# Kernel optimization log

Hardware: AMD Instinct MI355X
Metric: run time of the kernel (lower is better)

## Reference

```python
import jax, jax.numpy as jnp
import numpy as np

BN_EPS = 1e-5
LN_EPS = 1e-5


def conv1d(x, w, b):
    # x: (B, Cin, L), w: (Cout, Cin, K) 'same' padding
    pad = (w.shape[-1] - 1) // 2
    y = jax.lax.conv_general_dilated(x, w, (1,), [(pad, pad)],
                                     dimension_numbers=('NCH', 'OIH', 'NCH'))
    return y + b[None, :, None]


def bn_eval(x, g, b):
    # BatchNorm1d in eval mode with running_mean=0, running_var=1
    scale = g / np.float32(np.sqrt(1.0 + BN_EPS))
    return x * scale[None, :, None] + b[None, :, None]


def dss_kernel(lam_re, lam_im, log_dt, W_re, W_im, L):
    # lam_*: (N,), log_dt: (H,), W_*: (2, H, N) -> K: (2, H, L) real
    Lam = -jnp.exp(lam_re) + 1j * lam_im                  # (N,) stable poles
    dt = jnp.exp(log_dt)                                   # (H,)
    dtL = dt[:, None] * Lam[None, :]                       # (H, N)
    # ZOH-style input discretization folded into W
    Wc = (W_re + 1j * W_im) * ((jnp.exp(dtL) - 1.0) / Lam[None, :])[None]  # (2,H,N)
    pos = jnp.arange(L, dtype=jnp.float32)
    E = jnp.exp(dtL[:, :, None] * pos[None, None, :])      # (H, N, L) complex Vandermonde
    return jnp.einsum('chn,hnl->chl', Wc, E).real          # (2, H, L)


def dss_layer(x, lam_re, lam_im, log_dt, W_re, W_im, D, out_w, out_b):
    # x: (B, H, L) transposed DSS block, bidirectional, postact='glu'
    B, H, L = x.shape
    K = dss_kernel(lam_re, lam_im, log_dt, W_re, W_im, L)  # (2, H, L)
    zpad = jnp.zeros_like(K[0])
    k = (jnp.concatenate([K[0], zpad], -1) +
         jnp.concatenate([zpad, K[1][..., ::-1]], -1))     # (H, 2L) bidirectional kernel
    k_f = jnp.fft.rfft(k, axis=-1)                          # (H, L+1)
    u_f = jnp.fft.rfft(x, n=2 * L, axis=-1)                 # (B, H, L+1)
    y = jnp.fft.irfft(k_f[None] * u_f, n=2 * L, axis=-1)[..., :L]
    y = y + D[None, :, None] * x                            # skip term
    y = jax.nn.gelu(y, approximate=False)
    y = jnp.einsum('oh,bhl->bol', out_w, y) + out_b[None, :, None]  # (B, 2H, L)
    a, g = jnp.split(y, 2, axis=1)
    return a * jax.nn.sigmoid(g)                            # GLU -> (B, H, L)


def layernorm_ch(x, g, b):
    # LayerNorm over channel dim of (B, H, L)
    mu = x.mean(axis=1, keepdims=True)
    var = ((x - mu) ** 2).mean(axis=1, keepdims=True)
    return (x - mu) / jnp.sqrt(var + LN_EPS) * g[None, :, None] + b[None, :, None]


def reference(x, enc_w, enc_b, rn_w1, rn_b1, rn_g1, rn_be1, rn_w2, rn_b2, rn_g2,
              rn_be2, lam_re, lam_im, log_dt, W_re, W_im, D, out_w, out_b,
              ln_g, ln_b, dec_w, dec_b):
    x = conv1d(x, enc_w, enc_b)                             # (B, H, L)
    for i in range(rn_w1.shape[0]):                         # resnet L1Blocks
        z = jax.nn.relu(bn_eval(conv1d(x, rn_w1[i], rn_b1[i]), rn_g1[i], rn_be1[i]))
        z = bn_eval(conv1d(z, rn_w2[i], rn_b2[i]), rn_g2[i], rn_be2[i])
        x = jax.nn.relu(z + x)
    for i in range(lam_re.shape[0]):                        # DSS blocks (post-norm)
        z = dss_layer(x, lam_re[i], lam_im[i], log_dt[i], W_re[i], W_im[i],
                      D[i], out_w[i], out_b[i])
        x = layernorm_ch(z + x, ln_g[i], ln_b[i])
    return conv1d(x, dec_w, dec_b)                          # (B, d_output, L)


def setup_inputs() -> dict:
    key = jax.random.key(0)
    ks = jax.random.split(key, 12)
    B, L, H, N = 16, 8192, 128, 32
    nl, nr = 4, 3
    f = lambda k, shape, s=1.0: jax.random.normal(k, shape, dtype=jnp.float32) * np.float32(s)
    x = f(ks[0], (B, 5, L))
    enc_w = f(ks[1], (H, 5, 15), 1.0 / np.sqrt(5 * 15)); enc_b = jnp.zeros((H,), jnp.float32)
    rn_w1 = f(ks[2], (nr, H, H, 7), 1.0 / np.sqrt(H * 7)); rn_b1 = jnp.zeros((nr, H), jnp.float32)
    rn_w2 = f(ks[3], (nr, H, H, 7), 1.0 / np.sqrt(H * 7)); rn_b2 = jnp.zeros((nr, H), jnp.float32)
    rn_g1 = jnp.ones((nr, H), jnp.float32); rn_be1 = jnp.zeros((nr, H), jnp.float32)
    rn_g2 = jnp.ones((nr, H), jnp.float32); rn_be2 = jnp.zeros((nr, H), jnp.float32)
    lam_re = f(ks[4], (nl, N), 0.5)
    lam_im = jnp.pi * jnp.arange(N, dtype=jnp.float32)[None, :] * jnp.ones((nl, 1), jnp.float32)
    log_dt = f(ks[5], (nl, H), 0.5) - 4.0
    W_re = f(ks[6], (nl, 2, H, N), 1.0 / np.sqrt(N))
    W_im = f(ks[7], (nl, 2, H, N), 1.0 / np.sqrt(N))
    D = f(ks[8], (nl, H))
    out_w = f(ks[9], (nl, 2 * H, H), 1.0 / np.sqrt(H)); out_b = jnp.zeros((nl, 2 * H), jnp.float32)
    ln_g = jnp.ones((nl, H), jnp.float32); ln_b = jnp.zeros((nl, H), jnp.float32)
    dec_w = f(ks[10], (5, H, 15), 1.0 / np.sqrt(H * 15)); dec_b = jnp.zeros((5,), jnp.float32)
    return {'x': x, 'enc_w': enc_w, 'enc_b': enc_b, 'rn_w1': rn_w1, 'rn_b1': rn_b1,
            'rn_g1': rn_g1, 'rn_be1': rn_be1, 'rn_w2': rn_w2, 'rn_b2': rn_b2,
            'rn_g2': rn_g2, 'rn_be2': rn_be2, 'lam_re': lam_re, 'lam_im': lam_im,
            'log_dt': log_dt, 'W_re': W_re, 'W_im': W_im, 'D': D, 'out_w': out_w,
            'out_b': out_b, 'ln_g': ln_g, 'ln_b': ln_b, 'dec_w': dec_w, 'dec_b': dec_b}
```

## Files before the change

### kernel.cpp

```cpp
#include <hip/hip_runtime.h>
#include <hip/hip_bf16.h>


#define BN   16
#define HCH  128
#define LSEQ 8192
#define NST  32
#define NLAY 4
#define XT_BSTRIDE 2101248ull

typedef __attribute__((ext_vector_type(4))) float f32x4;
typedef __attribute__((ext_vector_type(8))) short short8;
typedef unsigned short u16;
typedef unsigned int   u32;

struct __align__(8) U2 { u32 x, y; };
struct __align__(16) US8 { u16 v[8]; };

__device__ __forceinline__ u16 f2bf(float f){
  union { float f; u32 u; } v; v.f = f;
  u32 u = v.u;
  return (u16)((u + 0x7fffu + ((u >> 16) & 1u)) >> 16);
}
__device__ __forceinline__ float bf2f(u32 lo16){
  union { u32 u; float f; } v; v.u = lo16 << 16; return v.f;
}
__device__ __forceinline__ float geluf(float v){
  return 0.5f * v * (1.0f + erff(v * 0.70710678118654752f));
}

#define GLDS16(g, l) \
  __builtin_amdgcn_global_load_lds((const __attribute__((address_space(1))) u32*)(g), \
                                   (__attribute__((address_space(3))) u32*)(l), 16, 0, 0)

__global__ void k_xpad(u16* xTs){
  int b = blockIdx.x, t = threadIdx.x;
  char* base = (char*)xTs + (size_t)b * XT_BSTRIDE;
  int r = t >> 4;
  int row = (r < 8) ? r : (8192 + r);
  f32x4 z = {0.f, 0.f, 0.f, 0.f};
  *(f32x4*)(base + (size_t)row * 256 + (size_t)(t & 15) * 16) = z;
}

__global__ void k_wxform(const float* __restrict__ w1, const float* __restrict__ w2, u16* __restrict__ wswz){
  int idx = blockIdx.x * 256 + threadIdx.x;
  if (idx >= 6 * 128 * 896) return;
  int conv = idx / (128 * 896);
  int rem  = idx % (128 * 896);
  int co = rem / 896, K = rem % 896;
  int k = K >> 7, ci = K & 127;
  const float* src = (conv & 1) ? w2 : w1;
  int blk = conv >> 1;
  float v = src[(((size_t)blk * 128 + co) * 128 + ci) * 7 + k];
  int chunk = K >> 6, j = K & 63;
  size_t byteoff = (size_t)conv * 229376 + (size_t)chunk * 16384 + (size_t)co * 128
                 + (u32)((j * 2) ^ ((co & 7) << 4));
  *(u16*)((char*)wswz + byteoff) = f2bf(v);
}

__global__ void k_wdec(const float* __restrict__ dw, u16* __restrict__ wd){
  int idx = blockIdx.x * 256 + threadIdx.x;
  if (idx >= 16 * 1920) return;
  int co = idx / 1920, K = idx % 1920;
  int k = K >> 7, ci = K & 127;
  float v = (co < 5) ? dw[((size_t)co * 128 + ci) * 15 + k] : 0.f;
  size_t byteoff = (size_t)co * 3840 + (u32)((K * 2) ^ ((co & 7) << 4));
  *(u16*)((char*)wd + byteoff) = f2bf(v);
}

__global__ void k_wglu(const float* __restrict__ ow, u16* __restrict__ wg){
  int idx = blockIdx.x * 256 + threadIdx.x;
  if (idx >= NLAY * 256 * 128) return;
  int layer = idx >> 15;
  int rem = idx & 32767;
  int q = rem >> 7, k = rem & 127;
  int row = (q & 1) ? (128 + (q >> 1)) : (q >> 1);
  float v = ow[((size_t)layer * 256 + row) * 128 + k];
  u16 hb = f2bf(v);
  u16 lb = f2bf(v - bf2f(hb));
  int a_hi = k >> 6, kk = k & 63;
  size_t base = (size_t)layer * 131072 + (size_t)q * 128 + (u32)((kk * 2) ^ ((q & 7) << 4));
  *(u16*)((char*)wg + base + (size_t)a_hi * 32768) = hb;
  *(u16*)((char*)wg + base + (size_t)(2 + a_hi) * 32768) = lb;
}

__global__ void k_dssprep(const float* __restrict__ lam_re, const float* __restrict__ lam_im,
                          const float* __restrict__ log_dt, const float* __restrict__ W_re,
                          const float* __restrict__ W_im, float* __restrict__ dssp){
  int idx = blockIdx.x * 256 + threadIdx.x;
  if (idx >= NLAY * HCH * NST) return;
  int layer = idx / (HCH * NST);
  int hn = idx % (HCH * NST);
  int h = hn / NST, n = hn % NST;
  float Lre = -expf(lam_re[layer * NST + n]);
  float Lim = lam_im[layer * NST + n];
  float dt  = expf(log_dt[layer * HCH + h]);
  float are = dt * Lre, aim = dt * Lim;
  float er = expf(are);
  float rre = er * cosf(aim);
  float rim = er * sinf(aim);
  float nre = rre - 1.f, nim = rim;
  float den = 1.f / (Lre * Lre + Lim * Lim);
  float fre = (nre * Lre + nim * Lim) * den;
  float fim = (nim * Lre - nre * Lim) * den;
  float* base = dssp + (size_t)layer * 6 * HCH * NST;
  base[(0 * HCH + h) * NST + n] = rre;
  base[(1 * HCH + h) * NST + n] = rim;
  #pragma unroll
  for (int cc = 0; cc < 2; ++cc){
    float wr_ = W_re[(((size_t)layer * 2 + cc) * HCH + h) * NST + n];
    float wi_ = W_im[(((size_t)layer * 2 + cc) * HCH + h) * NST + n];
    base[((2 + 2 * cc) * HCH + h) * NST + n] = wr_ * fre - wi_ * fim;
    base[((3 + 2 * cc) * HCH + h) * NST + n] = wr_ * fim + wi_ * fre;
  }
}

__global__ __launch_bounds__(256) void k_mats(const float* __restrict__ pp,
                                              u16* __restrict__ A1c, u16* __restrict__ A2c,
                                              float* __restrict__ rC){
  int h = blockIdx.x, t = threadIdx.x;
  __shared__ float pre[129][33], pim[129][33];
  __shared__ float w0re[32], w0im[32], w1re[32], w1im[32];
  __shared__ float tf[128], tb[128];
  if (t < 32){
    int n = t;
    float rre = pp[(0 * HCH + h) * NST + n], rim = pp[(1 * HCH + h) * NST + n];
    w0re[n] = pp[(2 * HCH + h) * NST + n]; w0im[n] = pp[(3 * HCH + h) * NST + n];
    w1re[n] = pp[(4 * HCH + h) * NST + n]; w1im[n] = pp[(5 * HCH + h) * NST + n];
    float pr = 1.f, pi = 0.f;
    pre[0][n] = 1.f; pim[0][n] = 0.f;
    for (int p = 1; p <= 128; ++p){
      float nr = pr * rre - pi * rim;
      float ni = pr * rim + pi * rre;
      pr = nr; pi = ni;
      pre[p][n] = pr; pim[p][n] = pi;
    }
    rC[h * 64 + 2 * n] = pr; rC[h * 64 + 2 * n + 1] = pi;
  }
  __syncthreads();
  if (t < 128){
    float s = 0.f;
    for (int n = 0; n < 32; ++n) s += w0re[n] * pre[t][n] - w0im[n] * pim[t][n];
    tf[t] = s;
  } else {
    int d = t - 128;
    if (d == 0) tb[0] = 0.f;
    else {
      float s = 0.f;
      for (int n = 0; n < 32; ++n) s += w1re[n] * pre[d - 1][n] - w1im[n] * pim[d - 1][n];
      tb[d] = s;
    }
  }
  __syncthreads();
  for (int idx = t; idx < 4 * 128 * 64; idx += 256){
    int a = idx >> 13, rem = idx & 8191, q = rem >> 6, k = rem & 63;
    int j = (a & 1) * 64 + k;
    int n, p; float wr_, wi_;
    if (q < 64){ n = q >> 1; p = 127 - j; wr_ = w0re[n]; wi_ = w0im[n]; }
    else       { n = (q - 64) >> 1; p = j; wr_ = w1re[n]; wi_ = w1im[n]; }
    float pr = pre[p][n], pi = pim[p][n];
    float v = (q & 1) ? (wr_ * pi + wi_ * pr) : (wr_ * pr - wi_ * pi);
    u16 hb = f2bf(v);
    u16 ob = (a < 2) ? hb : f2bf(v - bf2f(hb));
    *(u16*)((char*)A1c + (size_t)h * 65536 + (size_t)a * 16384 + (size_t)q * 128
            + (u32)((k * 2) ^ ((q & 7) << 4))) = ob;
  }
  for (int idx = t; idx < 8 * 128 * 64; idx += 256){
    int a = idx >> 13, rem = idx & 8191, i = rem >> 6, k = rem & 63;
    float v; bool lo;
    if (a < 4){
      int colT = (a & 1) * 64 + k;
      v = (i >= colT) ? tf[i - colT] : tb[colT - i];
      lo = (a >= 2);
    } else {
      int n = k >> 1;
      int p = (a < 6) ? (i + 1) : (127 - i);
      v = (k & 1) ? -pim[p][n] : pre[p][n];
      lo = (a == 5) || (a == 7);
    }
    u16 hb = f2bf(v);
    u16 ob = lo ? f2bf(v - bf2f(hb)) : hb;
    *(u16*)((char*)A2c + (size_t)h * 131072 + (size_t)a * 16384 + (size_t)i * 128
            + (u32)((k * 2) ^ ((i & 7) << 4))) = ob;
  }
}

__global__ __launch_bounds__(128) void k_enc(const float* __restrict__ xin, const float* __restrict__ w,
                                             const float* __restrict__ bias, float* __restrict__ X){
  int b = blockIdx.y, l0 = blockIdx.x * 64;
  int t = threadIdx.x;
  __shared__ float xs[5][78];
  for (int i = t; i < 5 * 78; i += 128){
    int ci = i / 78, j = i % 78;
    int l = l0 - 7 + j;
    xs[ci][j] = (l >= 0 && l < LSEQ) ? xin[((size_t)b * 5 + ci) * LSEQ + l] : 0.f;
  }
  float wreg[75];
  #pragma unroll
  for (int i = 0; i < 75; ++i) wreg[i] = w[t * 75 + i];
  float bc = bias[t];
  __syncthreads();
  size_t orow = ((size_t)b * HCH + t) * LSEQ + l0;
  for (int gb = 0; gb < 8; ++gb){
    float acc[8] = {0, 0, 0, 0, 0, 0, 0, 0};
    #pragma unroll
    for (int ci = 0; ci < 5; ++ci){
      #pragma unroll
      for (int k = 0; k < 15; ++k){
        float wv = wreg[ci * 15 + k];
        #pragma unroll
        for (int j = 0; j < 8; ++j)
          acc[j] = fmaf(wv, xs[ci][gb * 8 + j + k], acc[j]);
      }
    }
    f32x4 o0 = {acc[0] + bc, acc[1] + bc, acc[2] + bc, acc[3] + bc};
    f32x4 o1 = {acc[4] + bc, acc[5] + bc, acc[6] + bc, acc[7] + bc};
    *(f32x4*)&X[orow + gb * 8]     = o0;
    *(f32x4*)&X[orow + gb * 8 + 4] = o1;
  }
}

__global__ __launch_bounds__(256) void k_xform(const float* __restrict__ Xin, u16* __restrict__ xTs){
  int b = blockIdx.y, l0 = blockIdx.x * 64;
  int t = threadIdx.x;
  __shared__ float tile[128][65];
  #pragma unroll
  for (int it = 0; it < 32; ++it){
    int idx = t + it * 256;
    int ci = idx >> 6, j = idx & 63;
    tile[ci][j] = Xin[((size_t)b * HCH + ci) * LSEQ + l0 + j];
  }
  __syncthreads();
  int rl = t >> 2, q = t & 3;
  int l = l0 + rl;
  char* rowp = (char*)xTs + (size_t)b * XT_BSTRIDE + (size_t)(l + 8) * 256;
  u32 key = ((u32)l & 7u) << 4;
  #pragma unroll
  for (int ii = 0; ii < 8; ++ii){
    int c0 = q * 32 + ii * 4;
    U2 val;
    val.x = (u32)f2bf(tile[c0 + 0][rl]) | ((u32)f2bf(tile[c0 + 1][rl]) << 16);
    val.y = (u32)f2bf(tile[c0 + 2][rl]) | ((u32)f2bf(tile[c0 + 3][rl]) << 16);
    *(U2*)(rowp + (((u32)(c0 * 2)) ^ key)) = val;
  }
}

__global__ __launch_bounds__(256, 2) void k_conv(
    const u16* __restrict__ xTs, const u16* __restrict__ wcv,
    const float* __restrict__ bng, const float* __restrict__ bnb, const float* __restrict__ bnbe,
    const float* __restrict__ Xres, float* __restrict__ Xout)
{
  int b = blockIdx.y, l0 = blockIdx.x * 128;
  int tid = threadIdx.x, lane = tid & 63, wv = tid >> 6;
  int wr = wv >> 1, wc = wv & 1;
  int lan15 = lane & 15, lhi = lane >> 4;

  __shared__ alignas(16) u16 xt[144 * 128];
  __shared__ alignas(16) u16 wch[2][128 * 64];

  const char* xsrc = (const char*)xTs + (size_t)b * XT_BSTRIDE + (size_t)l0 * 256;
  #pragma unroll
  for (int is = 0; is < 9; ++is){
    int off = is * 4096 + wv * 1024;
    GLDS16(xsrc + off + (lane << 4), (char*)xt + off);
  }
  {
    const char* wsrc = (const char*)wcv;
    #pragma unroll
    for (int is = 0; is < 4; ++is){
      int off = is * 4096 + wv * 1024;
      GLDS16(wsrc + off + (lane << 4), (char*)&wch[0][0] + off);
    }
  }
  asm volatile("s_waitcnt vmcnt(0)" ::: "memory");
  __syncthreads();

  f32x4 acc[4][4];
  #pragma unroll
  for (int i = 0; i < 4; ++i)
    #pragma unroll
    for (int j = 0; j < 4; ++j) acc[i][j] = (f32x4){0.f, 0.f, 0.f, 0.f};

  for (int c = 0; c < 14; ++c){
    int cur = c & 1;
    if (c < 13){
      const char* wsrc = (const char*)wcv + (size_t)(c + 1) * 16384;
      #pragma unroll
      for (int is = 0; is < 4; ++is){
        int off = is * 4096 + wv * 1024;
        GLDS16(wsrc + off + (lane << 4), (char*)&wch[cur ^ 1][0] + off);
      }
    }
    int k = c >> 1;
    const char* wb = (const char*)&wch[cur][0];
    #pragma unroll
    for (int ks = 0; ks < 2; ++ks){
      short8 af[4], bf[4];
      int j0 = ks * 32 + lhi * 8;
      #pragma unroll
      for (int mt = 0; mt < 4; ++mt){
        int co = wr * 64 + mt * 16 + lan15;
        af[mt] = *(const short8*)(wb + co * 128 + ((j0 * 2) ^ ((co & 7) << 4)));
      }
      int ci0 = (c & 1) * 64 + ks * 32 + lhi * 8;
      #pragma unroll
      for (int nt = 0; nt < 4; ++nt){
        int ll = wc * 64 + nt * 16 + lan15;
        int row = ll + k + 5;
        int lg = l0 + ll + k - 3;
        bf[nt] = *(const short8*)((const char*)xt + row * 256 + ((ci0 * 2) ^ ((lg & 7) << 4)));
      }
      #pragma unroll
      for (int mt = 0; mt < 4; ++mt)
        #pragma unroll
        for (int nt = 0; nt < 4; ++nt)
          acc[mt][nt] = __builtin_amdgcn_mfma_f32_16x16x32_bf16(af[mt], bf[nt], acc[mt][nt], 0, 0, 0);
    }
    asm volatile("s_waitcnt vmcnt(0)" ::: "memory");
    __syncthreads();
  }

  bool hasres = (Xres != nullptr);
  #pragma unroll
  for (int mt = 0; mt < 4; ++mt){
    #pragma unroll
    for (int reg = 0; reg < 4; ++reg){
      int co = wr * 64 + mt * 16 + (lhi << 2) + reg;
      float A = bng[co] * 0.99999500003749968f;
      float Bc = fmaf(bnb[co], A, bnbe[co]);
      size_t rowb = ((size_t)b * HCH + co) * LSEQ;
      #pragma unroll
      for (int nt = 0; nt < 4; ++nt){
        int l = l0 + wc * 64 + nt * 16 + lan15;
        float v = fmaf(acc[mt][nt][reg], A, Bc);
        if (hasres) v += Xres[rowb + l];
        v = fmaxf(v, 0.f);
        Xout[rowb + l] = v;
      }
    }
  }
}

__device__ __forceinline__ void stage_x_tile(const float* __restrict__ X, int h, int ct,
                                             char* xh, char* xl, int t){
  int k8 = t & 15;
  int c0 = t >> 4;
  #pragma unroll
  for (int it = 0; it < 8; ++it){
    int col = c0 + it * 16;
    int c = ct * 8 + (col >> 4), b = col & 15;
    const float* src = X + ((size_t)b * HCH + h) * LSEQ + (size_t)c * 128 + k8 * 8;
    f32x4 v0 = *(const f32x4*)src;
    f32x4 v1 = *(const f32x4*)(src + 4);
    US8 hi, lo;
    #pragma unroll
    for (int e = 0; e < 4; ++e){
      u16 hb = f2bf(v0[e]);
      hi.v[e] = hb; lo.v[e] = f2bf(v0[e] - bf2f(hb));
      u16 hb2 = f2bf(v1[e]);
      hi.v[e + 4] = hb2; lo.v[e + 4] = f2bf(v1[e] - bf2f(hb2));
    }
    u32 off = (u32)col * 256 + (u32)((k8 * 16) ^ ((col & 7) << 4));
    *(US8*)(xh + off) = hi;
    *(US8*)(xl + off) = lo;
  }
}

__global__ __launch_bounds__(256) void k_dss1(const float* __restrict__ X,
                                              const u16* __restrict__ A1c,
                                              float* __restrict__ P){
  int ct = blockIdx.x, h = blockIdx.y;
  int tid = threadIdx.x, lane = tid & 63, wv = tid >> 6;
  int wr = wv >> 1, wc = wv & 1, lan15 = lane & 15, lhi = lane >> 4;
  __shared__ alignas(16) u16 bx[32768];
  __shared__ alignas(16) u16 ach[2][8192];

  stage_x_tile(X, h, ct, (char*)bx, (char*)bx + 32768, tid);
  const char* abase = (const char*)A1c + (size_t)h * 65536;
  #pragma unroll
  for (int is = 0; is < 4; ++is){
    int off = is * 4096 + wv * 1024;
    GLDS16(abase + off + (lane << 4), (char*)&ach[0][0] + off);
  }
  asm volatile("s_waitcnt vmcnt(0)" ::: "memory");
  __syncthreads();

  f32x4 acc[4][4];
  #pragma unroll
  for (int i = 0; i < 4; ++i)
    #pragma unroll
    for (int j = 0; j < 4; ++j) acc[i][j] = (f32x4){0.f, 0.f, 0.f, 0.f};

  const int asel[6] = {0, 1, 0, 1, 2, 3};
  const int bsel[6] = {0, 0, 1, 1, 0, 0};
  const int bk0 [6] = {0, 64, 0, 64, 0, 64};
  #pragma unroll
  for (int s = 0; s < 6; ++s){
    if (s < 5){
      const char* an = abase + (size_t)asel[s + 1] * 16384;
      #pragma unroll
      for (int is = 0; is < 4; ++is){
        int off = is * 4096 + wv * 1024;
        GLDS16(an + off + (lane << 4), (char*)&ach[(s + 1) & 1][0] + off);
      }
    }
    const char* bt = (const char*)bx + bsel[s] * 32768;
    const char* at = (const char*)&ach[s & 1][0];
    #pragma unroll
    for (int ks = 0; ks < 2; ++ks){
      int ka = ks * 32 + lhi * 8;
      short8 af[4], bf[4];
      #pragma unroll
      for (int mt = 0; mt < 4; ++mt){
        int q = wr * 64 + mt * 16 + lan15;
        af[mt] = *(const short8*)(at + q * 128 + ((ka * 2) ^ ((q & 7) << 4)));
      }
      int kb = bk0[s] + ka;
      #pragma unroll
      for (int nt = 0; nt < 4; ++nt){
        int col = wc * 64 + nt * 16 + lan15;
        bf[nt] = *(const short8*)(bt + col * 256 + ((kb * 2) ^ ((col & 7) << 4)));
      }
      #pragma unroll
      for (int mt = 0; mt < 4; ++mt)
        #pragma unroll
        for (int nt = 0; nt < 4; ++nt)
          acc[mt][nt] = __builtin_amdgcn_mfma_f32_16x16x32_bf16(af[mt], bf[nt], acc[mt][nt], 0, 0, 0);
    }
    asm volatile("s_waitcnt vmcnt(0)" ::: "memory");
    __syncthreads();
  }

  #pragma unroll
  for (int mt = 0; mt < 4; ++mt)
    #pragma unroll
    for (int nt = 0; nt < 4; ++nt){
      int col = ct * 128 + wc * 64 + nt * 16 + lan15;
      int q0 = wr * 64 + mt * 16 + (lhi << 2);
      *(f32x4*)&P[((size_t)h * 1024 + col) * 128 + q0] = acc[mt][nt];
    }
}

__global__ __launch_bounds__(256) void k_scan(const float* __restrict__ P,
                                              const float* __restrict__ rC,
                                              u16* __restrict__ Sf, u16* __restrict__ Sb){
  int part = blockIdx.x & 3, h = blockIdx.x >> 2;
  int t = threadIdx.x;
  int dir = part >> 1;
  int b = (part & 1) * 8 + (t >> 5);
  int n = t & 31;
  float rre = rC[h * 64 + 2 * n], rim = rC[h * 64 + 2 * n + 1];
  u16* SO = dir ? Sb : Sf;
  const float* pbase = P + (size_t)h * 131072 + (size_t)b * 128 + dir * 64 + 2 * n;
  float sre = 0.f, sim = 0.f;
  u32 key = ((u32)b & 7u) << 4;
  for (int ii = 0; ii < 64; ++ii){
    int c = dir ? (63 - ii) : ii;
    u16 hr = f2bf(sre), hm = f2bf(sim);
    u32 hw = (u32)hr | ((u32)hm << 16);
    u32 lw = (u32)f2bf(sre - bf2f(hr)) | ((u32)f2bf(sim - bf2f(hm)) << 16);
    char* sp = (char*)SO + ((size_t)(h * 8 + (c >> 3)) * 2) * 16384
             + (size_t)((c & 7) * 16 + b) * 128 + (u32)((4 * n) ^ key);
    *(u32*)sp = hw;
    *(u32*)(sp + 16384) = lw;
    const float* pp = pbase + (size_t)c * 2048;
    float pr = pp[0], pi = pp[1];
    float nr = rre * sre - rim * sim + pr;
    float ni = rre * sim + rim * sre + pi;
    sre = nr; sim = ni;
  }
}

__global__ __launch_bounds__(256) void k_dss2(const float* __restrict__ X,
                                              const u16* __restrict__ A2c,
                                              const u16* __restrict__ Sf,
                                              const u16* __restrict__ Sb,
                                              const float* __restrict__ Dv,
                                              float* __restrict__ G){
  int ct = blockIdx.x, h = blockIdx.y;
  int tid = threadIdx.x, lane = tid & 63, wv = tid >> 6;
  int wr = wv >> 1, wc = wv & 1, lan15 = lane & 15, lhi = lane >> 4;
  __shared__ alignas(16) u16 bx[32768];
  __shared__ alignas(16) u16 ach[2][8192];

  stage_x_tile(X, h, ct, (char*)bx, (char*)bx + 32768, tid);
  const char* abase = (const char*)A2c + (size_t)h * 131072;
  #pragma unroll
  for (int is = 0; is < 4; ++is){
    int off = is * 4096 + wv * 1024;
    GLDS16(abase + off + (lane << 4), (char*)&ach[0][0] + off);
  }
  asm volatile("s_waitcnt vmcnt(0)" ::: "memory");
  __syncthreads();

  f32x4 acc[4][4];
  #pragma unroll
  for (int i = 0; i < 4; ++i)
    #pragma unroll
    for (int j = 0; j < 4; ++j) acc[i][j] = (f32x4){0.f, 0.f, 0.f, 0.f};

  {
    const int asel[6] = {0, 1, 0, 1, 2, 3};
    const int bsel[6] = {0, 0, 1, 1, 0, 0};
    const int bk0 [6] = {0, 64, 0, 64, 0, 64};
    #pragma unroll
    for (int s = 0; s < 6; ++s){
      if (s < 5){
        const char* an = abase + (size_t)asel[s + 1] * 16384;
        #pragma unroll
        for (int is = 0; is < 4; ++is){
          int off = is * 4096 + wv * 1024;
          GLDS16(an + off + (lane << 4), (char*)&ach[(s + 1) & 1][0] + off);
        }
      }
      const char* bt = (const char*)bx + bsel[s] * 32768;
      const char* at = (const char*)&ach[s & 1][0];
      #pragma unroll
      for (int ks = 0; ks < 2; ++ks){
        int ka = ks * 32 + lhi * 8;
        short8 af[4], bf[4];
        #pragma unroll
        for (int mt = 0; mt < 4; ++mt){
          int i = wr * 64 + mt * 16 + lan15;
          af[mt] = *(const short8*)(at + i * 128 + ((ka * 2) ^ ((i & 7) << 4)));
        }
        int kb = bk0[s] + ka;
        #pragma unroll
        for (int nt = 0; nt < 4; ++nt){
          int col = wc * 64 + nt * 16 + lan15;
          bf[nt] = *(const short8*)(bt + col * 256 + ((kb * 2) ^ ((col & 7) << 4)));
        }
        #pragma unroll
        for (int mt = 0; mt < 4; ++mt)
          #pragma unroll
          for (int nt = 0; nt < 4; ++nt)
            acc[mt][nt] = __builtin_amdgcn_mfma_f32_16x16x32_bf16(af[mt], bf[nt], acc[mt][nt], 0, 0, 0);
      }
      asm volatile("s_waitcnt vmcnt(0)" ::: "memory");
      __syncthreads();
    }
  }
  {
    const char* st0 = (const char*)Sf + ((size_t)(h * 8 + ct) * 2) * 16384;
    const char* st2 = (const char*)Sb + ((size_t)(h * 8 + ct) * 2) * 16384;
    const char* stile[4] = {st0, st0 + 16384, st2, st2 + 16384};
    #pragma unroll
    for (int tt = 0; tt < 4; ++tt){
      #pragma unroll
      for (int is = 0; is < 4; ++is){
        int off = is * 4096 + wv * 1024;
        GLDS16(stile[tt] + off + (lane << 4), (char*)bx + tt * 16384 + off);
      }
    }
    const char* an = abase + 4 * 16384;
    #pragma unroll
    for (int is = 0; is < 4; ++is){
      int off = is * 4096 + wv * 1024;
      GLDS16(an + off + (lane << 4), (char*)&ach[0][0] + off);
    }
    asm volatile("s_waitcnt vmcnt(0)" ::: "memory");
    __syncthreads();
  }
  {
    const int asel[6] = {4, 4, 5, 6, 6, 7};
    const int bof [6] = {0, 16384, 0, 32768, 49152, 32768};
    #pragma unroll
    for (int s = 0; s < 6; ++s){
      if (s < 5){
        const char* an = abase + (size_t)asel[s + 1] * 16384;
        #pragma unroll
        for (int is = 0; is < 4; ++is){
          int off = is * 4096 + wv * 1024;
          GLDS16(an + off + (lane << 4), (char*)&ach[(s + 1) & 1][0] + off);
        }
      }
      const char* bt = (const char*)bx + bof[s];
      const char* at = (const char*)&ach[s & 1][0];
      #pragma unroll
      for (int ks = 0; ks < 2; ++ks){
        int ka = ks * 32 + lhi * 8;
        short8 af[4], bf[4];
        #pragma unroll
        for (int mt = 0; mt < 4; ++mt){
          int i = wr * 64 + mt * 16 + lan15;
          af[mt] = *(const short8*)(at + i * 128 + ((ka * 2) ^ ((i & 7) << 4)));
        }
        #pragma unroll
        for (int nt = 0; nt < 4; ++nt){
          int col = wc * 64 + nt * 16 + lan15;
          bf[nt] = *(const short8*)(bt + col * 128 + ((ka * 2) ^ ((col & 7) << 4)));
        }
        #pragma unroll
        for (int mt = 0; mt < 4; ++mt)
          #pragma unroll
          for (int nt = 0; nt < 4; ++nt)
            acc[mt][nt] = __builtin_amdgcn_mfma_f32_16x16x32_bf16(af[mt], bf[nt], acc[mt][nt], 0, 0, 0);
      }
      asm volatile("s_waitcnt vmcnt(0)" ::: "memory");
      __syncthreads();
    }
  }
  float Dh = Dv[h];
  #pragma unroll
  for (int mt = 0; mt < 4; ++mt)
    #pragma unroll
    for (int nt = 0; nt < 4; ++nt){
      int col = wc * 64 + nt * 16 + lan15;
      int c = ct * 8 + (col >> 4), b = col & 15;
      int i0 = wr * 64 + mt * 16 + (lhi << 2);
      size_t base = ((size_t)b * HCH + h) * LSEQ + (size_t)c * 128 + i0;
      f32x4 xv = *(const f32x4*)&X[base];
      f32x4 ov;
      #pragma unroll
      for (int e = 0; e < 4; ++e)
        ov[e] = geluf(acc[mt][nt][e] + Dh * xv[e]);
      *(f32x4*)&G[base] = ov;
    }
}

__global__ __launch_bounds__(256) void k_glu2(
    const float* __restrict__ G,
    const u16* __restrict__ Wg,
    const float* __restrict__ ob,
    const float* __restrict__ lng, const float* __restrict__ lnb,
    float* __restrict__ X)
{
  int b = blockIdx.y, l0 = blockIdx.x * 64;
  int tid = threadIdx.x, lane = tid & 63, wv = tid >> 6;
  int lan15 = lane & 15, lhi = lane >> 4;
  __shared__ alignas(16) u16 gt[2][64 * 128];
  __shared__ alignas(16) u16 ach[256 * 64];
  __shared__ float lnbuf[4][64][2];

  {
    int hp = tid & 63, lgrp = tid >> 6;
    const float* g0 = G + ((size_t)b * HCH + 2 * hp) * LSEQ + l0 + lgrp * 16;
    const float* g1 = g0 + LSEQ;
    #pragma unroll
    for (int j4 = 0; j4 < 4; ++j4){
      f32x4 r0 = *(const f32x4*)(g0 + j4 * 4);
      f32x4 r1 = *(const f32x4*)(g1 + j4 * 4);
      #pragma unroll
      for (int e = 0; e < 4; ++e){
        int l = lgrp * 16 + j4 * 4 + e;
        u16 h0 = f2bf(r0[e]), h1 = f2bf(r1[e]);
        u16 q0 = f2bf(r0[e] - bf2f(h0)), q1 = f2bf(r1[e] - bf2f(h1));
        u32 off = (u32)l * 256 + (((u32)hp * 4) ^ (((u32)l & 7u) << 4));
        *(u32*)((char*)&gt[0][0] + off) = (u32)h0 | ((u32)h1 << 16);
        *(u32*)((char*)&gt[1][0] + off) = (u32)q0 | ((u32)q1 << 16);
      }
    }
  }

  f32x4 acc[4][4];
  #pragma unroll
  for (int i = 0; i < 4; ++i)
    #pragma unroll
    for (int j = 0; j < 4; ++j) acc[i][j] = (f32x4){0.f, 0.f, 0.f, 0.f};

  const int asel[6] = {0, 1, 0, 1, 2, 3};
  const int bsel[6] = {0, 0, 1, 1, 0, 0};
  const int bk0 [6] = {0, 64, 0, 64, 0, 64};
  for (int s = 0; s < 6; ++s){
    __syncthreads();
    const char* an = (const char*)Wg + (size_t)asel[s] * 32768;
    #pragma unroll
    for (int is = 0; is < 8; ++is){
      int off = is * 4096 + wv * 1024;
      GLDS16(an + off + (lane << 4), (char*)ach + off);
    }
    asm volatile("s_waitcnt vmcnt(0)" ::: "memory");
    __syncthreads();
    const char* bt = (const char*)&gt[bsel[s]][0];
    #pragma unroll
    for (int ks = 0; ks < 2; ++ks){
      int ka = ks * 32 + lhi * 8;
      short8 af[4], bf[4];
      #pragma unroll
      for (int mt = 0; mt < 4; ++mt){
        int q = wv * 64 + mt * 16 + lan15;
        af[mt] = *(const short8*)((const char*)ach + q * 128 + ((ka * 2) ^ ((q & 7) << 4)));
      }
      int kb = bk0[s] + ka;
      #pragma unroll
      for (int nt = 0; nt < 4; ++nt){
        int col = nt * 16 + lan15;
        bf[nt] = *(const short8*)(bt + col * 256 + ((kb * 2) ^ ((col & 7) << 4)));
      }
      #pragma unroll
      for (int mt = 0; mt < 4; ++mt)
        #pragma unroll
        for (int nt = 0; nt < 4; ++nt)
          acc[mt][nt] = __builtin_amdgcn_mfma_f32_16x16x32_bf16(af[mt], bf[nt], acc[mt][nt], 0, 0, 0);
    }
  }

  float s1v[4] = {0, 0, 0, 0}, s2v[4] = {0, 0, 0, 0};
  float oba[4][2], obg[4][2];
  #pragma unroll
  for (int mt = 0; mt < 4; ++mt)
    #pragma unroll
    for (int e = 0; e < 2; ++e){
      int o = wv * 32 + mt * 8 + lhi * 2 + e;
      oba[mt][e] = ob[o]; obg[mt][e] = ob[o + 128];
    }
  #pragma unroll
  for (int nt = 0; nt < 4; ++nt){
    int l = l0 + nt * 16 + lan15;
    #pragma unroll
    for (int mt = 0; mt < 4; ++mt){
      #pragma unroll
      for (int e = 0; e < 2; ++e){
        int o = wv * 32 + mt * 8 + lhi * 2 + e;
        float a = acc[mt][nt][2 * e]     + oba[mt][e];
        float g = acc[mt][nt][2 * e + 1] + obg[mt][e];
        float z = a * (1.f / (1.f + expf(-g)));
        float u = z + X[((size_t)b * HCH + o) * LSEQ + l];
        acc[mt][nt][2 * e] = u;
        s1v[nt] += u; s2v[nt] += u * u;
      }
    }
  }
  #pragma unroll
  for (int nt = 0; nt < 4; ++nt){
    s1v[nt] += __shfl_xor(s1v[nt], 16, 64);
    s1v[nt] += __shfl_xor(s1v[nt], 32, 64);
    s2v[nt] += __shfl_xor(s2v[nt], 16, 64);
    s2v[nt] += __shfl_xor(s2v[nt], 32, 64);
  }
  if (lhi == 0){
    #pragma unroll
    for (int nt = 0; nt < 4; ++nt){
      lnbuf[wv][nt * 16 + lan15][0] = s1v[nt];
      lnbuf[wv][nt * 16 + lan15][1] = s2v[nt];
    }
  }
  __syncthreads();
  #pragma unroll
  for (int nt = 0; nt < 4; ++nt){
    int col = nt * 16 + lan15;
    float S1 = lnbuf[0][col][0] + lnbuf[1][col][0] + lnbuf[2][col][0] + lnbuf[3][col][0];
    float S2 = lnbuf[0][col][1] + lnbuf[1][col][1] + lnbuf[2][col][1] + lnbuf[3][col][1];
    float mu = S1 * (1.f / 128.f);
    float var = S2 * (1.f / 128.f) - mu * mu;
    float rs = rsqrtf(var + 1e-5f);
    int l = l0 + col;
    #pragma unroll
    for (int mt = 0; mt < 4; ++mt)
      #pragma unroll
      for (int e = 0; e < 2; ++e){
        int o = wv * 32 + mt * 8 + lhi * 2 + e;
        float u = acc[mt][nt][2 * e];
        X[((size_t)b * HCH + o) * LSEQ + l] = (u - mu) * rs * lng[o] + lnb[o];
      }
  }
}

__global__ __launch_bounds__(256, 1) void k_dec2(const u16* __restrict__ xTs, const u16* __restrict__ wd,
                                                 const float* __restrict__ bias, float* __restrict__ out){
  int b = blockIdx.y, l0 = blockIdx.x * 128;
  int tid = threadIdx.x, lane = tid & 63, wv = tid >> 6;
  int lan15 = lane & 15, lhi = lane >> 4;
  __shared__ alignas(16) u16 xt[144 * 128];
  __shared__ alignas(16) u16 ws[16 * 1920];
  const char* xsrc = (const char*)xTs + (size_t)b * XT_BSTRIDE + (size_t)l0 * 256;
  #pragma unroll
  for (int is = 0; is < 9; ++is){
    int off = is * 4096 + wv * 1024;
    GLDS16(xsrc + off + (lane << 4), (char*)xt + off);
  }
  #pragma unroll
  for (int is = 0; is < 15; ++is){
    int off = is * 4096 + wv * 1024;
    GLDS16((const char*)wd + off + (lane << 4), (char*)ws + off);
  }
  asm volatile("s_waitcnt vmcnt(0)" ::: "memory");
  __syncthreads();
  f32x4 acc[2] = {(f32x4){0, 0, 0, 0}, (f32x4){0, 0, 0, 0}};
  for (int k = 0; k < 15; ++k){
    #pragma unroll
    for (int ks = 0; ks < 4; ++ks){
      int K = k * 128 + ks * 32 + lhi * 8;
      short8 af = *(const short8*)((const char*)ws + lan15 * 3840 + (((u32)(K * 2)) ^ (((u32)lan15 & 7u) << 4)));
      #pragma unroll
      for (int nt = 0; nt < 2; ++nt){
        int ll = wv * 32 + nt * 16 + lan15;
        int lg = l0 + ll + k - 7;
        int row = ll + k + 1;
        short8 bf = *(const short8*)((const char*)xt + row * 256 + ((((ks * 32 + lhi * 8) * 2)) ^ ((lg & 7) << 4)));
        acc[nt] = __builtin_amdgcn_mfma_f32_16x16x32_bf16(af, bf, acc[nt], 0, 0, 0);
      }
    }
  }
  #pragma unroll
  for (int nt = 0; nt < 2; ++nt){
    int l = l0 + wv * 32 + nt * 16 + lan15;
    #pragma unroll
    for (int reg = 0; reg < 4; ++reg){
      int co = (lhi << 2) + reg;
      if (co < 5) out[((size_t)b * 5 + co) * LSEQ + l] = acc[nt][reg] + bias[co];
    }
  }
}

extern "C" void kernel_launch(void* const* d_in, const int* in_sizes, int n_in,
                              void* d_out, int out_size, void* d_ws, size_t ws_size,
                              hipStream_t stream){
  (void)in_sizes; (void)n_in; (void)out_size; (void)ws_size;
  const float* x_in   = (const float*)d_in[0];
  const float* enc_w  = (const float*)d_in[1];
  const float* enc_b  = (const float*)d_in[2];
  const float* rn_w1  = (const float*)d_in[3];
  const float* rn_b1  = (const float*)d_in[4];
  const float* rn_g1  = (const float*)d_in[5];
  const float* rn_be1 = (const float*)d_in[6];
  const float* rn_w2  = (const float*)d_in[7];
  const float* rn_b2  = (const float*)d_in[8];
  const float* rn_g2  = (const float*)d_in[9];
  const float* rn_be2 = (const float*)d_in[10];
  const float* lam_re = (const float*)d_in[11];
  const float* lam_im = (const float*)d_in[12];
  const float* log_dt = (const float*)d_in[13];
  const float* W_re   = (const float*)d_in[14];
  const float* W_im   = (const float*)d_in[15];
  const float* Dv     = (const float*)d_in[16];
  const float* out_w  = (const float*)d_in[17];
  const float* out_b  = (const float*)d_in[18];
  const float* ln_g   = (const float*)d_in[19];
  const float* ln_b   = (const float*)d_in[20];
  const float* dec_w  = (const float*)d_in[21];
  const float* dec_b  = (const float*)d_in[22];

  char* ws = (char*)d_ws;
  float* X    = (float*)(ws + 0ull);
  float* PG   = (float*)(ws + 67108864ull);
  u16*   Sf   = (u16*)  (ws + 134217728ull);
  u16*   Sb   = (u16*)  (ws + 167772160ull);
  u16*   xTs  = (u16*)  (ws + 134217728ull);
  u16*   A1c  = (u16*)  (ws + 201326592ull);
  u16*   A2c  = (u16*)  (ws + 209715200ull);
  u16*   wswz = (u16*)  (ws + 226492416ull);
  u16*   wdec = (u16*)  (ws + 227868672ull);
  float* dssp = (float*)(ws + 227930112ull);
  float* rC   = (float*)(ws + 228323328ull);
  u16*   wglu = (u16*)  (ws + 228356096ull);

  k_xpad<<<16, 256, 0, stream>>>(xTs);
  k_wxform<<<2688, 256, 0, stream>>>(rn_w1, rn_w2, wswz);
  k_wdec<<<120, 256, 0, stream>>>(dec_w, wdec);
  k_wglu<<<512, 256, 0, stream>>>(out_w, wglu);
  k_dssprep<<<64, 256, 0, stream>>>(lam_re, lam_im, log_dt, W_re, W_im, dssp);
  k_enc<<<dim3(128, 16), 128, 0, stream>>>(x_in, enc_w, enc_b, X);

  for (int r = 0; r < 3; ++r){
    k_xform<<<dim3(128, 16), 256, 0, stream>>>(X, xTs);
    k_conv<<<dim3(64, 16), 256, 0, stream>>>(xTs, (const u16*)((char*)wswz + (size_t)(2 * r) * 229376),
        rn_g1 + r * HCH, rn_b1 + r * HCH, rn_be1 + r * HCH, nullptr, PG);
    k_xform<<<dim3(128, 16), 256, 0, stream>>>(PG, xTs);
    k_conv<<<dim3(64, 16), 256, 0, stream>>>(xTs, (const u16*)((char*)wswz + (size_t)(2 * r + 1) * 229376),
        rn_g2 + r * HCH, rn_b2 + r * HCH, rn_be2 + r * HCH, X, X);
  }
  for (int dl = 0; dl < NLAY; ++dl){
    k_mats<<<128, 256, 0, stream>>>(dssp + (size_t)dl * 6 * HCH * NST, A1c, A2c, rC);
    k_dss1<<<dim3(8, 128), 256, 0, stream>>>(X, A1c, PG);
    k_scan<<<512, 256, 0, stream>>>(PG, rC, Sf, Sb);
    k_dss2<<<dim3(8, 128), 256, 0, stream>>>(X, A2c, Sf, Sb, Dv + dl * HCH, PG);
    k_glu2<<<dim3(128, 16), 256, 0, stream>>>(PG, (const u16*)((char*)wglu + (size_t)dl * 131072),
        out_b + dl * 256, ln_g + dl * HCH, ln_b + dl * HCH, X);
  }
  k_xpad<<<16, 256, 0, stream>>>(xTs);
  k_xform<<<dim3(128, 16), 256, 0, stream>>>(X, xTs);
  k_dec2<<<dim3(64, 16), 256, 0, stream>>>(xTs, wdec, dec_b, (float*)d_out);
}
```

Measured before the change: 1.744 ms.

## Fuse bf16 transpose into conv epilogue, restructure DSS GEMM staging and grid order

```diff
diff --git a/kernel.cpp b/kernel.cpp
--- a/kernel.cpp
+++ b/kernel.cpp
@@ -16,6 +16,7 @@
 
 struct __align__(8) U2 { u32 x, y; };
 struct __align__(16) US8 { u16 v[8]; };
+struct __align__(8) US4 { u16 v[4]; };
 
 __device__ __forceinline__ u16 f2bf(float f){
   union { float f; u32 u; } v; v.f = f;
@@ -248,7 +249,7 @@
 __global__ __launch_bounds__(256, 2) void k_conv(
     const u16* __restrict__ xTs, const u16* __restrict__ wcv,
     const float* __restrict__ bng, const float* __restrict__ bnb, const float* __restrict__ bnbe,
-    const float* __restrict__ Xres, float* __restrict__ Xout)
+    const float* __restrict__ Xres, float* __restrict__ Xout, u16* __restrict__ xTsOut)
 {
   int b = blockIdx.y, l0 = blockIdx.x * 128;
   int tid = threadIdx.x, lane = tid & 63, wv = tid >> 6;
@@ -321,23 +322,41 @@
   }
 
   bool hasres = (Xres != nullptr);
+  bool hasout = (Xout != nullptr);
+  u16* tr = xt;
   #pragma unroll
   for (int mt = 0; mt < 4; ++mt){
+    float A4[4], B4[4];
+    int co0 = wr * 64 + mt * 16 + (lhi << 2);
     #pragma unroll
     for (int reg = 0; reg < 4; ++reg){
-      int co = wr * 64 + mt * 16 + (lhi << 2) + reg;
-      float A = bng[co] * 0.99999500003749968f;
-      float Bc = fmaf(bnb[co], A, bnbe[co]);
-      size_t rowb = ((size_t)b * HCH + co) * LSEQ;
-      #pragma unroll
-      for (int nt = 0; nt < 4; ++nt){
-        int l = l0 + wc * 64 + nt * 16 + lan15;
-        float v = fmaf(acc[mt][nt][reg], A, Bc);
-        if (hasres) v += Xres[rowb + l];
+      A4[reg] = bng[co0 + reg] * 0.99999500003749968f;
+      B4[reg] = fmaf(bnb[co0 + reg], A4[reg], bnbe[co0 + reg]);
+    }
+    #pragma unroll
+    for (int nt = 0; nt < 4; ++nt){
+      int ll = wc * 64 + nt * 16 + lan15;
+      int l = l0 + ll;
+      US4 o;
+      #pragma unroll
+      for (int reg = 0; reg < 4; ++reg){
+        float v = fmaf(acc[mt][nt][reg], A4[reg], B4[reg]);
+        if (hasres) v += Xres[((size_t)b * HCH + co0 + reg) * LSEQ + l];
         v = fmaxf(v, 0.f);
-        Xout[rowb + l] = v;
-      }
-    }
+        if (hasout) Xout[((size_t)b * HCH + co0 + reg) * LSEQ + l] = v;
+        o.v[reg] = f2bf(v);
+      }
+      *(US4*)((char*)tr + ll * 256 + (u32)((co0 * 2) ^ ((ll & 7) << 4))) = o;
+    }
+  }
+  if (xTsOut){
+    __syncthreads();
+    int row = tid >> 1, half = tid & 1;
+    const char* s = (const char*)tr + row * 256 + half * 128;
+    char* d = (char*)xTsOut + (size_t)b * XT_BSTRIDE + (size_t)(l0 + row + 8) * 256 + half * 128;
+    #pragma unroll
+    for (int i = 0; i < 8; ++i)
+      *(f32x4*)(d + i * 16) = *(const f32x4*)(s + i * 16);
   }
 }
 
@@ -369,21 +388,14 @@
 __global__ __launch_bounds__(256) void k_dss1(const float* __restrict__ X,
                                               const u16* __restrict__ A1c,
                                               float* __restrict__ P){
-  int ct = blockIdx.x, h = blockIdx.y;
+  int h = blockIdx.x, ct = blockIdx.y;
   int tid = threadIdx.x, lane = tid & 63, wv = tid >> 6;
   int wr = wv >> 1, wc = wv & 1, lan15 = lane & 15, lhi = lane >> 4;
   __shared__ alignas(16) u16 bx[32768];
-  __shared__ alignas(16) u16 ach[2][8192];
+  __shared__ alignas(16) u16 ach[8192];
 
   stage_x_tile(X, h, ct, (char*)bx, (char*)bx + 32768, tid);
   const char* abase = (const char*)A1c + (size_t)h * 65536;
-  #pragma unroll
-  for (int is = 0; is < 4; ++is){
-    int off = is * 4096 + wv * 1024;
-    GLDS16(abase + off + (lane << 4), (char*)&ach[0][0] + off);
-  }
-  asm volatile("s_waitcnt vmcnt(0)" ::: "memory");
-  __syncthreads();
 
   f32x4 acc[4][4];
   #pragma unroll
@@ -391,44 +403,43 @@
     #pragma unroll
     for (int j = 0; j < 4; ++j) acc[i][j] = (f32x4){0.f, 0.f, 0.f, 0.f};
 
-  const int asel[6] = {0, 1, 0, 1, 2, 3};
-  const int bsel[6] = {0, 0, 1, 1, 0, 0};
-  const int bk0 [6] = {0, 64, 0, 64, 0, 64};
-  #pragma unroll
-  for (int s = 0; s < 6; ++s){
-    if (s < 5){
-      const char* an = abase + (size_t)asel[s + 1] * 16384;
-      #pragma unroll
-      for (int is = 0; is < 4; ++is){
-        int off = is * 4096 + wv * 1024;
-        GLDS16(an + off + (lane << 4), (char*)&ach[(s + 1) & 1][0] + off);
-      }
-    }
-    const char* bt = (const char*)bx + bsel[s] * 32768;
-    const char* at = (const char*)&ach[s & 1][0];
-    #pragma unroll
-    for (int ks = 0; ks < 2; ++ks){
-      int ka = ks * 32 + lhi * 8;
-      short8 af[4], bf[4];
-      #pragma unroll
-      for (int mt = 0; mt < 4; ++mt){
-        int q = wr * 64 + mt * 16 + lan15;
-        af[mt] = *(const short8*)(at + q * 128 + ((ka * 2) ^ ((q & 7) << 4)));
-      }
-      int kb = bk0[s] + ka;
-      #pragma unroll
-      for (int nt = 0; nt < 4; ++nt){
-        int col = wc * 64 + nt * 16 + lan15;
-        bf[nt] = *(const short8*)(bt + col * 256 + ((kb * 2) ^ ((col & 7) << 4)));
-      }
-      #pragma unroll
-      for (int mt = 0; mt < 4; ++mt)
-        #pragma unroll
-        for (int nt = 0; nt < 4; ++nt)
-          acc[mt][nt] = __builtin_amdgcn_mfma_f32_16x16x32_bf16(af[mt], bf[nt], acc[mt][nt], 0, 0, 0);
+  #pragma unroll
+  for (int g = 0; g < 4; ++g){
+    __syncthreads();
+    const char* an = abase + (size_t)g * 16384;
+    #pragma unroll
+    for (int is = 0; is < 4; ++is){
+      int off = is * 4096 + wv * 1024;
+      GLDS16(an + off + (lane << 4), (char*)ach + off);
     }
     asm volatile("s_waitcnt vmcnt(0)" ::: "memory");
     __syncthreads();
+    int kb0 = (g & 1) * 64;
+    int npass = (g < 2) ? 2 : 1;
+    for (int p = 0; p < npass; ++p){
+      const char* bt = (const char*)bx + p * 32768;
+      #pragma unroll
+      for (int ks = 0; ks < 2; ++ks){
+        int ka = ks * 32 + lhi * 8;
+        short8 af[4], bf[4];
+        #pragma unroll
+        for (int mt = 0; mt < 4; ++mt){
+          int q = wr * 64 + mt * 16 + lan15;
+          af[mt] = *(const short8*)((const char*)ach + q * 128 + ((ka * 2) ^ ((q & 7) << 4)));
+        }
+        int kb = kb0 + ka;
+        #pragma unroll
+        for (int nt = 0; nt < 4; ++nt){
+          int col = wc * 64 + nt * 16 + lan15;
+          bf[nt] = *(const short8*)(bt + col * 256 + ((kb * 2) ^ ((col & 7) << 4)));
+        }
+        #pragma unroll
+        for (int mt = 0; mt < 4; ++mt)
+          #pragma unroll
+          for (int nt = 0; nt < 4; ++nt)
+            acc[mt][nt] = __builtin_amdgcn_mfma_f32_16x16x32_bf16(af[mt], bf[nt], acc[mt][nt], 0, 0, 0);
+      }
+    }
   }
 
   #pragma unroll
@@ -477,44 +488,89 @@
                                               const u16* __restrict__ Sb,
                                               const float* __restrict__ Dv,
                                               float* __restrict__ G){
-  int ct = blockIdx.x, h = blockIdx.y;
+  int h = blockIdx.x, ct = blockIdx.y;
   int tid = threadIdx.x, lane = tid & 63, wv = tid >> 6;
   int wr = wv >> 1, wc = wv & 1, lan15 = lane & 15, lhi = lane >> 4;
   __shared__ alignas(16) u16 bx[32768];
-  __shared__ alignas(16) u16 ach[2][8192];
-
+  __shared__ alignas(16) u16 ach[8192];
+
+  {
+    const char* st0 = (const char*)Sf + ((size_t)(h * 8 + ct) * 2) * 16384;
+    const char* st2 = (const char*)Sb + ((size_t)(h * 8 + ct) * 2) * 16384;
+    const char* stile[4] = {st0, st0 + 16384, st2, st2 + 16384};
+    #pragma unroll
+    for (int tt = 0; tt < 4; ++tt){
+      #pragma unroll
+      for (int is = 0; is < 4; ++is){
+        int off = is * 4096 + wv * 1024;
+        GLDS16(stile[tt] + off + (lane << 4), (char*)bx + tt * 16384 + off);
+      }
+    }
+  }
+  const char* abase = (const char*)A2c + (size_t)h * 131072;
+
+  f32x4 acc[4][4];
+  #pragma unroll
+  for (int i = 0; i < 4; ++i)
+    #pragma unroll
+    for (int j = 0; j < 4; ++j) acc[i][j] = (f32x4){0.f, 0.f, 0.f, 0.f};
+
+  {
+    const int bo0[4] = {0, 0, 32768, 32768};
+    #pragma unroll
+    for (int g = 0; g < 4; ++g){
+      __syncthreads();
+      const char* an = abase + (size_t)(4 + g) * 16384;
+      #pragma unroll
+      for (int is = 0; is < 4; ++is){
+        int off = is * 4096 + wv * 1024;
+        GLDS16(an + off + (lane << 4), (char*)ach + off);
+      }
+      asm volatile("s_waitcnt vmcnt(0)" ::: "memory");
+      __syncthreads();
+      int npass = (g & 1) ? 1 : 2;
+      for (int p = 0; p < npass; ++p){
+        const char* bt = (const char*)bx + bo0[g] + p * 16384;
+        #pragma unroll
+        for (int ks = 0; ks < 2; ++ks){
+          int ka = ks * 32 + lhi * 8;
+          short8 af[4], bf[4];
+          #pragma unroll
+          for (int mt = 0; mt < 4; ++mt){
+            int i = wr * 64 + mt * 16 + lan15;
+            af[mt] = *(const short8*)((const char*)ach + i * 128 + ((ka * 2) ^ ((i & 7) << 4)));
+          }
+          #pragma unroll
+          for (int nt = 0; nt < 4; ++nt){
+            int col = wc * 64 + nt * 16 + lan15;
+            bf[nt] = *(const short8*)(bt + col * 128 + ((ka * 2) ^ ((col & 7) << 4)));
+          }
+          #pragma unroll
+          for (int mt = 0; mt < 4; ++mt)
+            #pragma unroll
+            for (int nt = 0; nt < 4; ++nt)
+              acc[mt][nt] = __builtin_amdgcn_mfma_f32_16x16x32_bf16(af[mt], bf[nt], acc[mt][nt], 0, 0, 0);
+        }
+      }
+    }
+  }
+  __syncthreads();
   stage_x_tile(X, h, ct, (char*)bx, (char*)bx + 32768, tid);
-  const char* abase = (const char*)A2c + (size_t)h * 131072;
-  #pragma unroll
-  for (int is = 0; is < 4; ++is){
-    int off = is * 4096 + wv * 1024;
-    GLDS16(abase + off + (lane << 4), (char*)&ach[0][0] + off);
-  }
-  asm volatile("s_waitcnt vmcnt(0)" ::: "memory");
-  __syncthreads();
-
-  f32x4 acc[4][4];
-  #pragma unroll
-  for (int i = 0; i < 4; ++i)
-    #pragma unroll
-    for (int j = 0; j < 4; ++j) acc[i][j] = (f32x4){0.f, 0.f, 0.f, 0.f};
-
-  {
-    const int asel[6] = {0, 1, 0, 1, 2, 3};
-    const int bsel[6] = {0, 0, 1, 1, 0, 0};
-    const int bk0 [6] = {0, 64, 0, 64, 0, 64};
-    #pragma unroll
-    for (int s = 0; s < 6; ++s){
-      if (s < 5){
-        const char* an = abase + (size_t)asel[s + 1] * 16384;
-        #pragma unroll
-        for (int is = 0; is < 4; ++is){
-          int off = is * 4096 + wv * 1024;
-          GLDS16(an + off + (lane << 4), (char*)&ach[(s + 1) & 1][0] + off);
-        }
-      }
-      const char* bt = (const char*)bx + bsel[s] * 32768;
-      const char* at = (const char*)&ach[s & 1][0];
+  #pragma unroll
+  for (int g = 0; g < 4; ++g){
+    __syncthreads();
+    const char* an = abase + (size_t)g * 16384;
+    #pragma unroll
+    for (int is = 0; is < 4; ++is){
+      int off = is * 4096 + wv * 1024;
+      GLDS16(an + off + (lane << 4), (char*)ach + off);
+    }
+    asm volatile("s_waitcnt vmcnt(0)" ::: "memory");
+    __syncthreads();
+    int kb0 = (g & 1) * 64;
+    int npass = (g < 2) ? 2 : 1;
+    for (int p = 0; p < npass; ++p){
+      const char* bt = (const char*)bx + p * 32768;
       #pragma unroll
       for (int ks = 0; ks < 2; ++ks){
         int ka = ks * 32 + lhi * 8;
@@ -522,9 +578,9 @@
         #pragma unroll
         for (int mt = 0; mt < 4; ++mt){
           int i = wr * 64 + mt * 16 + lan15;
-          af[mt] = *(const short8*)(at + i * 128 + ((ka * 2) ^ ((i & 7) << 4)));
+          af[mt] = *(const short8*)((const char*)ach + i * 128 + ((ka * 2) ^ ((i & 7) << 4)));
         }
-        int kb = bk0[s] + ka;
+        int kb = kb0 + ka;
         #pragma unroll
         for (int nt = 0; nt < 4; ++nt){
           int col = wc * 64 + nt * 16 + lan15;
@@ -536,68 +592,6 @@
           for (int nt = 0; nt < 4; ++nt)
             acc[mt][nt] = __builtin_amdgcn_mfma_f32_16x16x32_bf16(af[mt], bf[nt], acc[mt][nt], 0, 0, 0);
       }
-      asm volatile("s_waitcnt vmcnt(0)" ::: "memory");
-      __syncthreads();
-    }
-  }
-  {
-    const char* st0 = (const char*)Sf + ((size_t)(h * 8 + ct) * 2) * 16384;
-    const char* st2 = (const char*)Sb + ((size_t)(h * 8 + ct) * 2) * 16384;
-    const char* stile[4] = {st0, st0 + 16384, st2, st2 + 16384};
-    #pragma unroll
-    for (int tt = 0; tt < 4; ++tt){
-      #pragma unroll
-      for (int is = 0; is < 4; ++is){
-        int off = is * 4096 + wv * 1024;
-        GLDS16(stile[tt] + off + (lane << 4), (char*)bx + tt * 16384 + off);
-      }
-    }
-    const char* an = abase + 4 * 16384;
-    #pragma unroll
-    for (int is = 0; is < 4; ++is){
-      int off = is * 4096 + wv * 1024;
-      GLDS16(an + off + (lane << 4), (char*)&ach[0][0] + off);
-    }
-    asm volatile("s_waitcnt vmcnt(0)" ::: "memory");
-    __syncthreads();
-  }
-  {
-    const int asel[6] = {4, 4, 5, 6, 6, 7};
-    const int bof [6] = {0, 16384, 0, 32768, 49152, 32768};
-    #pragma unroll
-    for (int s = 0; s < 6; ++s){
-      if (s < 5){
-        const char* an = abase + (size_t)asel[s + 1] * 16384;
-        #pragma unroll
-        for (int is = 0; is < 4; ++is){
-          int off = is * 4096 + wv * 1024;
-          GLDS16(an + off + (lane << 4), (char*)&ach[(s + 1) & 1][0] + off);
-        }
-      }
-      const char* bt = (const char*)bx + bof[s];
-      const char* at = (const char*)&ach[s & 1][0];
-      #pragma unroll
-      for (int ks = 0; ks < 2; ++ks){
-        int ka = ks * 32 + lhi * 8;
-        short8 af[4], bf[4];
-        #pragma unroll
-        for (int mt = 0; mt < 4; ++mt){
-          int i = wr * 64 + mt * 16 + lan15;
-          af[mt] = *(const short8*)(at + i * 128 + ((ka * 2) ^ ((i & 7) << 4)));
-        }
-        #pragma unroll
-        for (int nt = 0; nt < 4; ++nt){
-          int col = wc * 64 + nt * 16 + lan15;
-          bf[nt] = *(const short8*)(bt + col * 128 + ((ka * 2) ^ ((col & 7) << 4)));
-        }
-        #pragma unroll
-        for (int mt = 0; mt < 4; ++mt)
-          #pragma unroll
-          for (int nt = 0; nt < 4; ++nt)
-            acc[mt][nt] = __builtin_amdgcn_mfma_f32_16x16x32_bf16(af[mt], bf[nt], acc[mt][nt], 0, 0, 0);
-      }
-      asm volatile("s_waitcnt vmcnt(0)" ::: "memory");
-      __syncthreads();
     }
   }
   float Dh = Dv[h];
@@ -608,12 +602,16 @@
       int col = wc * 64 + nt * 16 + lan15;
       int c = ct * 8 + (col >> 4), b = col & 15;
       int i0 = wr * 64 + mt * 16 + (lhi << 2);
+      u32 off = (u32)col * 256 + (u32)((2 * i0) ^ ((col & 7) << 4));
+      US4 hx = *(const US4*)((const char*)bx + off);
+      US4 lx = *(const US4*)((const char*)bx + 32768 + off);
       size_t base = ((size_t)b * HCH + h) * LSEQ + (size_t)c * 128 + i0;
-      f32x4 xv = *(const f32x4*)&X[base];
       f32x4 ov;
       #pragma unroll
-      for (int e = 0; e < 4; ++e)
-        ov[e] = geluf(acc[mt][nt][e] + Dh * xv[e]);
+      for (int e = 0; e < 4; ++e){
+        float xv = bf2f(hx.v[e]) + bf2f(lx.v[e]);
+        ov[e] = geluf(acc[mt][nt][e] + Dh * xv);
+      }
       *(f32x4*)&G[base] = ov;
     }
 }
@@ -834,9 +832,10 @@
   char* ws = (char*)d_ws;
   float* X    = (float*)(ws + 0ull);
   float* PG   = (float*)(ws + 67108864ull);
+  u16*   xTsB = (u16*)  (ws + 67108864ull);
   u16*   Sf   = (u16*)  (ws + 134217728ull);
   u16*   Sb   = (u16*)  (ws + 167772160ull);
-  u16*   xTs  = (u16*)  (ws + 134217728ull);
+  u16*   xTsA = (u16*)  (ws + 134217728ull);
   u16*   A1c  = (u16*)  (ws + 201326592ull);
   u16*   A2c  = (u16*)  (ws + 209715200ull);
   u16*   wswz = (u16*)  (ws + 226492416ull);
@@ -845,30 +844,30 @@
   float* rC   = (float*)(ws + 228323328ull);
   u16*   wglu = (u16*)  (ws + 228356096ull);
 
-  k_xpad<<<16, 256, 0, stream>>>(xTs);
+  k_xpad<<<16, 256, 0, stream>>>(xTsA);
+  k_xpad<<<16, 256, 0, stream>>>(xTsB);
   k_wxform<<<2688, 256, 0, stream>>>(rn_w1, rn_w2, wswz);
   k_wdec<<<120, 256, 0, stream>>>(dec_w, wdec);
   k_wglu<<<512, 256, 0, stream>>>(out_w, wglu);
   k_dssprep<<<64, 256, 0, stream>>>(lam_re, lam_im, log_dt, W_re, W_im, dssp);
   k_enc<<<dim3(128, 16), 128, 0, stream>>>(x_in, enc_w, enc_b, X);
+  k_xform<<<dim3(128, 16), 256, 0, stream>>>(X, xTsA);
 
   for (int r = 0; r < 3; ++r){
-    k_xform<<<dim3(128, 16), 256, 0, stream>>>(X, xTs);
-    k_conv<<<dim3(64, 16), 256, 0, stream>>>(xTs, (const u16*)((char*)wswz + (size_t)(2 * r) * 229376),
-        rn_g1 + r * HCH, rn_b1 + r * HCH, rn_be1 + r * HCH, nullptr, PG);
-    k_xform<<<dim3(128, 16), 256, 0, stream>>>(PG, xTs);
-    k_conv<<<dim3(64, 16), 256, 0, stream>>>(xTs, (const u16*)((char*)wswz + (size_t)(2 * r + 1) * 229376),
-        rn_g2 + r * HCH, rn_b2 + r * HCH, rn_be2 + r * HCH, X, X);
+    k_conv<<<dim3(64, 16), 256, 0, stream>>>(xTsA, (const u16*)((char*)wswz + (size_t)(2 * r) * 229376),
+        rn_g1 + r * HCH, rn_b1 + r * HCH, rn_be1 + r * HCH, nullptr, nullptr, xTsB);
+    k_conv<<<dim3(64, 16), 256, 0, stream>>>(xTsB, (const u16*)((char*)wswz + (size_t)(2 * r + 1) * 229376),
+        rn_g2 + r * HCH, rn_b2 + r * HCH, rn_be2 + r * HCH, X, X, (r == 2) ? nullptr : xTsA);
   }
   for (int dl = 0; dl < NLAY; ++dl){
     k_mats<<<128, 256, 0, stream>>>(dssp + (size_t)dl * 6 * HCH * NST, A1c, A2c, rC);
-    k_dss1<<<dim3(8, 128), 256, 0, stream>>>(X, A1c, PG);
+    k_dss1<<<dim3(128, 8), 256, 0, stream>>>(X, A1c, PG);
     k_scan<<<512, 256, 0, stream>>>(PG, rC, Sf, Sb);
-    k_dss2<<<dim3(8, 128), 256, 0, stream>>>(X, A2c, Sf, Sb, Dv + dl * HCH, PG);
+    k_dss2<<<dim3(128, 8), 256, 0, stream>>>(X, A2c, Sf, Sb, Dv + dl * HCH, PG);
     k_glu2<<<dim3(128, 16), 256, 0, stream>>>(PG, (const u16*)((char*)wglu + (size_t)dl * 131072),
         out_b + dl * 256, ln_g + dl * HCH, ln_b + dl * HCH, X);
   }
-  k_xpad<<<16, 256, 0, stream>>>(xTs);
-  k_xform<<<dim3(128, 16), 256, 0, stream>>>(X, xTs);
-  k_dec2<<<dim3(64, 16), 256, 0, stream>>>(xTs, wdec, dec_b, (float*)d_out);
-}
+  k_xpad<<<16, 256, 0, stream>>>(xTsA);
+  k_xform<<<dim3(128, 16), 256, 0, stream>>>(X, xTsA);
+  k_dec2<<<dim3(64, 16), 256, 0, stream>>>(xTsA, wdec, dec_b, (float*)d_out);
+}
```

Result: faster. 1.472 ms (-15.6%).
